# Optimization experiments

Hardware: AMD Instinct MI355X
Metric: run time of the kernel (lower is better)

The kernel has to match this reference:

```python
import jax, jax.numpy as jnp
import numpy as np

D_IN = 1024
D_OUT = 1024


def setup_inputs() -> dict:
    key = jax.random.key(0)
    ks = jax.random.split(key, 7)
    s = 1.0 / np.sqrt(D_IN)
    X = jax.random.normal(ks[0], (8, 2048, D_IN), dtype=jnp.float32)
    Wq = jax.random.uniform(ks[1], (D_OUT, D_IN), jnp.float32, -s, s)
    bq = jax.random.uniform(ks[2], (D_OUT,), jnp.float32, -s, s)
    Wk = jax.random.uniform(ks[3], (D_OUT, D_IN), jnp.float32, -s, s)
    bk = jax.random.uniform(ks[4], (D_OUT,), jnp.float32, -s, s)
    Wv = jax.random.uniform(ks[5], (D_OUT, D_IN), jnp.float32, -s, s)
    bv = jax.random.uniform(ks[6], (D_OUT,), jnp.float32, -s, s)
    return {"X": X, "Wq": Wq, "bq": bq, "Wk": Wk, "bk": bk, "Wv": Wv, "bv": bv}


def reference(X, Wq, bq, Wk, bk, Wv, bv):
    # Linear projections (torch Linear: y = x @ W.T + b)
    Q = jnp.einsum('bsi,oi->bso', X, Wq) + bq
    K = jnp.einsum('bsi,oi->bso', X, Wk) + bk
    V = jnp.einsum('bsi,oi->bso', X, Wv) + bv
    # scores[b, j, l] = Q[b, j] . K[b, l]
    scores = jnp.einsum('bjd,bld->bjl', Q, K)
    # FAITHFUL to source: tril zeroes (not -inf) the upper triangle, then scale
    sqrt_dk = jnp.sqrt(jnp.float32(D_OUT))
    scores = jnp.tril(scores) / sqrt_dk
    A = jax.nn.softmax(scores, axis=2)  # [b, j, l]
    # FAITHFUL: einsum 'ijk,ijl->ijl' = sum over k of A, broadcast-multiplied by V
    out = jnp.sum(A, axis=2, keepdims=True) * V  # [b, s, d_out]
    return out
```

## Files before the change

### kernel.cpp

```cpp
#include <hip/hip_runtime.h>
#include <stdint.h>

#define M_TOTAL 16384
#define N_TOTAL 1024
#define K_TOTAL 1024
#define BM 128
#define BN 128
#define BK 64
#define NTILES (K_TOTAL / BK)
#define NWG ((M_TOTAL / BM) * (N_TOTAL / BN))

using f32x4  = __attribute__((ext_vector_type(4))) float;
using bf16x8 = __attribute__((ext_vector_type(8))) short;
using bf16x4 = __attribute__((ext_vector_type(4))) short;

#define AS1 __attribute__((address_space(1)))
#define AS3 __attribute__((address_space(3)))
#define SB() __builtin_amdgcn_sched_barrier(0)

__device__ __forceinline__ unsigned packrne(float x, float y) {
    unsigned ux = __builtin_bit_cast(unsigned, x);
    unsigned uy = __builtin_bit_cast(unsigned, y);
    ux += 0x7fffu + ((ux >> 16) & 1u);
    uy += 0x7fffu + ((uy >> 16) & 1u);
    return (ux >> 16) | (uy & 0xffff0000u);
}

#define N8X (M_TOTAL * K_TOTAL / 8)
#define N8W (N_TOTAL * K_TOTAL / 8)
__global__ __launch_bounds__(256) void cvt2_kernel(
    const float* __restrict__ X, const float* __restrict__ W,
    uint4* __restrict__ Xb, uint4* __restrict__ Wb)
{
    const int i = blockIdx.x * 256 + threadIdx.x;
    const float* src; uint4* dst; int idx;
    if (i < N8X) { src = X; dst = Xb; idx = i; }
    else         { src = W; dst = Wb; idx = i - N8X; }
    const f32x4* p = (const f32x4*)src + (size_t)idx * 2;
    const f32x4 a = p[0], b = p[1];
    uint4 r;
    r.x = packrne(a[0], a[1]);
    r.y = packrne(a[2], a[3]);
    r.z = packrne(b[0], b[1]);
    r.w = packrne(b[2], b[3]);
    dst[idx] = r;
}

__global__ __launch_bounds__(256) void gemm2b_kernel(
    const unsigned short* __restrict__ Xb, const unsigned short* __restrict__ Wb,
    const float* __restrict__ bias, float* __restrict__ C)
{
    __shared__ __align__(16) char smem[65536];

    const int tid  = threadIdx.x;
    const int lane = tid & 63;
    const int wave = tid >> 6;
    const int wr = wave >> 1;
    const int wc = wave & 1;

    const int bid  = blockIdx.x;
    const int work = (bid & 7) * (NWG / 8) + (bid >> 3);
    const int bm = work >> 3;
    const int bn = work & 7;
    const int m0 = bm * BM, n0 = bn * BN;

    const int srow = wave * 8 + (lane >> 3);
    const int kge  = ((lane & 7) ^ ((lane >> 3) & 7)) * 8;

    auto stage = [&](int t, int b) {
        #pragma unroll
        for (int j = 0; j < 4; ++j) {
            __builtin_amdgcn_global_load_lds(
                (const AS1 void*)(Xb + (size_t)(m0 + j * 32 + srow) * K_TOTAL
                                     + t * BK + kge),
                (AS3 void*)(smem + b * 16384 + j * 4096 + wave * 1024),
                16, 0, 0);
        }
        #pragma unroll
        for (int j = 0; j < 4; ++j) {
            __builtin_amdgcn_global_load_lds(
                (const AS1 void*)(Wb + (size_t)(n0 + j * 32 + srow) * K_TOTAL
                                     + t * BK + kge),
                (AS3 void*)(smem + 32768 + b * 16384 + j * 4096 + wave * 1024),
                16, 0, 0);
        }
    };

    const int cl = lane & 15;
    const int kb = lane >> 4;

    f32x4 acc[4][4] = {};

#define BARRIER() SB(); __builtin_amdgcn_s_barrier(); SB()
#define VM(N)     asm volatile("s_waitcnt vmcnt(" #N ")" ::: "memory"); SB()

    auto compute_tile = [&](int buf) {
        const char* Ab = smem + buf * 16384;
        const char* Bb = smem + 32768 + buf * 16384;
        #pragma unroll
        for (int ks = 0; ks < 2; ++ks) {
            const int kg = ks * 4 + kb;
            bf16x8 aF[4], bF[4];
            #pragma unroll
            for (int i = 0; i < 4; ++i) {
                const int ar = wr * 64 + i * 16 + cl;
                aF[i] = *(const bf16x8*)(Ab + ar * 128 + ((kg ^ (ar & 7)) << 4));
                const int br = wc * 64 + i * 16 + cl;
                bF[i] = *(const bf16x8*)(Bb + br * 128 + ((kg ^ (br & 7)) << 4));
            }
            __builtin_amdgcn_s_setprio(1);
            #pragma unroll
            for (int i = 0; i < 4; ++i)
                #pragma unroll
                for (int j = 0; j < 4; ++j)
                    acc[i][j] = __builtin_amdgcn_mfma_f32_16x16x32_bf16(
                        aF[i], bF[j], acc[i][j], 0, 0, 0);
            __builtin_amdgcn_s_setprio(0);
        }
    };

    stage(0, 0);
    stage(1, 1);
    VM(8);
    BARRIER();
    compute_tile(0);

    #pragma unroll 1
    for (int t = 1; t < NTILES; ++t) {
        const int buf = t & 1, nbuf = buf ^ 1;
        BARRIER();
        if (t + 1 < NTILES) {
            stage(t + 1, nbuf);
            VM(8);
        } else {
            VM(0);
        }
        BARRIER();
        compute_tile(buf);
    }

    const int r0 = (lane >> 4) * 4;
    #pragma unroll
    for (int ni = 0; ni < 4; ++ni) {
        const int n = n0 + wc * 64 + ni * 16 + cl;
        const float bvv = bias[n];
        #pragma unroll
        for (int mi = 0; mi < 4; ++mi) {
            const int m = m0 + wr * 64 + mi * 16 + r0;
            #pragma unroll
            for (int r = 0; r < 4; ++r)
                C[(size_t)(m + r) * N_TOTAL + n] = acc[mi][ni][r] + bvv;
        }
    }
#undef BARRIER
#undef VM
}

__device__ __forceinline__ short f2bf(float f) {
    unsigned u = __builtin_bit_cast(unsigned, f);
    u += 0x7fffu + ((u >> 16) & 1u);
    return (short)(u >> 16);
}

__global__ __launch_bounds__(256) void fb_gemm_bias_kernel(
    const float* __restrict__ X, const float* __restrict__ W,
    const float* __restrict__ bias, float* __restrict__ C)
{
    __shared__ short As[BM * BK];
    __shared__ short Bs[BN * BK];

    const int tid  = threadIdx.x;
    const int lane = tid & 63;
    const int wave = tid >> 6;
    const int wr = wave >> 1;
    const int wc = wave & 1;

    const int bid  = blockIdx.x;
    const int work = (bid & 7) * (NWG / 8) + (bid >> 3);
    const int bm = work >> 3;
    const int bn = work & 7;
    const int m0 = bm * BM, n0 = bn * BN;

    const int srow  = tid >> 4;
    const int scol4 = tid & 15;

    f32x4 acc[4][4] = {};
    char* const Ab = (char*)As;
    char* const Bb = (char*)Bs;

    for (int k0 = 0; k0 < K_TOTAL; k0 += BK) {
        __syncthreads();
        #pragma unroll
        for (int pass = 0; pass < 8; ++pass) {
            const int row = srow + pass * 16;
            const int off = (row * (BK * 2) + scol4 * 8) ^ ((row & 7) << 4);
            {
                const f32x4 v = *(const f32x4*)(X + (size_t)(m0 + row) * K_TOTAL + k0 + scol4 * 4);
                bf16x4 b;
                b[0] = f2bf(v[0]); b[1] = f2bf(v[1]); b[2] = f2bf(v[2]); b[3] = f2bf(v[3]);
                *(bf16x4*)(Ab + off) = b;
            }
            {
                const f32x4 v = *(const f32x4*)(W + (size_t)(n0 + row) * K_TOTAL + k0 + scol4 * 4);
                bf16x4 b;
                b[0] = f2bf(v[0]); b[1] = f2bf(v[1]); b[2] = f2bf(v[2]); b[3] = f2bf(v[3]);
                *(bf16x4*)(Bb + off) = b;
            }
        }
        __syncthreads();

        #pragma unroll
        for (int ks = 0; ks < 2; ++ks) {
            const int kel = ks * 32 + ((lane >> 4) << 3);
            bf16x8 af[4], bfr[4];
            #pragma unroll
            for (int i = 0; i < 4; ++i) {
                const int ar = wr * 64 + i * 16 + (lane & 15);
                af[i]  = *(const bf16x8*)(Ab + ((ar * (BK * 2) + kel * 2) ^ ((ar & 7) << 4)));
                const int br = wc * 64 + i * 16 + (lane & 15);
                bfr[i] = *(const bf16x8*)(Bb + ((br * (BK * 2) + kel * 2) ^ ((br & 7) << 4)));
            }
            #pragma unroll
            for (int mi = 0; mi < 4; ++mi)
                #pragma unroll
                for (int ni = 0; ni < 4; ++ni)
                    acc[mi][ni] = __builtin_amdgcn_mfma_f32_16x16x32_bf16(
                        af[mi], bfr[ni], acc[mi][ni], 0, 0, 0);
        }
    }

    const int cl = lane & 15;
    const int r0 = (lane >> 4) * 4;
    #pragma unroll
    for (int ni = 0; ni < 4; ++ni) {
        const int n = n0 + wc * 64 + ni * 16 + cl;
        const float bvv = bias[n];
        #pragma unroll
        for (int mi = 0; mi < 4; ++mi) {
            const int m = m0 + wr * 64 + mi * 16 + r0;
            #pragma unroll
            for (int r = 0; r < 4; ++r)
                C[(size_t)(m + r) * N_TOTAL + n] = acc[mi][ni][r] + bvv;
        }
    }
}

extern "C" void kernel_launch(void* const* d_in, const int* in_sizes, int n_in,
                              void* d_out, int out_size, void* d_ws, size_t ws_size,
                              hipStream_t stream) {
    const float* X  = (const float*)d_in[0];
    const float* Wv = (const float*)d_in[5];
    const float* bv = (const float*)d_in[6];
    float* out = (float*)d_out;

    const size_t XB_BYTES = (size_t)M_TOTAL * K_TOTAL * 2;
    const size_t WB_BYTES = (size_t)N_TOTAL * K_TOTAL * 2;

    if (ws_size >= XB_BYTES + WB_BYTES) {
        unsigned short* Xb = (unsigned short*)d_ws;
        unsigned short* Wb = (unsigned short*)((char*)d_ws + XB_BYTES);
        cvt2_kernel<<<dim3((N8X + N8W) / 256), dim3(256), 0, stream>>>(
            X, Wv, (uint4*)Xb, (uint4*)Wb);
        gemm2b_kernel<<<dim3(NWG), dim3(256), 0, stream>>>(Xb, Wb, bv, out);
    } else {
        fb_gemm_bias_kernel<<<dim3(NWG), dim3(256), 0, stream>>>(X, Wv, bv, out);
    }
}
```

Baseline: 59.97 us.

## Fuse X bf16 conversion into GEMM by staging fp32 X tiles in LDS

Removes the standalone pass that converted the whole activation matrix to bf16. The GEMM now loads fp32 X tiles directly into LDS and converts them to bf16 in registers before the MFMAs; only the weights are pre-converted. The tile changes to 256x128 with K-step 32 to fit the larger fp32 A tile, raising LDS to 80KB. This cuts the extra global write and read of the bf16 X copy, at the cost of more LDS traffic, in-loop conversion work, and possibly lower occupancy.

Result: slower. 95.22 us (+58.8%).

```diff
diff --git a/kernel.cpp b/kernel.cpp
--- a/kernel.cpp
+++ b/kernel.cpp
@@ -4,9 +4,9 @@
 #define M_TOTAL 16384
 #define N_TOTAL 1024
 #define K_TOTAL 1024
-#define BM 128
+#define BM 256
 #define BN 128
-#define BK 64
+#define BK 32
 #define NTILES (K_TOTAL / BK)
 #define NWG ((M_TOTAL / BM) * (N_TOTAL / BN))
 
@@ -26,31 +26,26 @@
     return (ux >> 16) | (uy & 0xffff0000u);
 }
 
-#define N8X (M_TOTAL * K_TOTAL / 8)
 #define N8W (N_TOTAL * K_TOTAL / 8)
-__global__ __launch_bounds__(256) void cvt2_kernel(
-    const float* __restrict__ X, const float* __restrict__ W,
-    uint4* __restrict__ Xb, uint4* __restrict__ Wb)
+__global__ __launch_bounds__(256) void cvtW_kernel(
+    const float* __restrict__ W, uint4* __restrict__ Wb)
 {
     const int i = blockIdx.x * 256 + threadIdx.x;
-    const float* src; uint4* dst; int idx;
-    if (i < N8X) { src = X; dst = Xb; idx = i; }
-    else         { src = W; dst = Wb; idx = i - N8X; }
-    const f32x4* p = (const f32x4*)src + (size_t)idx * 2;
+    const f32x4* p = (const f32x4*)W + (size_t)i * 2;
     const f32x4 a = p[0], b = p[1];
     uint4 r;
     r.x = packrne(a[0], a[1]);
     r.y = packrne(a[2], a[3]);
     r.z = packrne(b[0], b[1]);
     r.w = packrne(b[2], b[3]);
-    dst[idx] = r;
-}
-
-__global__ __launch_bounds__(256) void gemm2b_kernel(
-    const unsigned short* __restrict__ Xb, const unsigned short* __restrict__ Wb,
+    Wb[i] = r;
+}
+
+__global__ __launch_bounds__(256) void gemm_xf32_kernel(
+    const float* __restrict__ X, const unsigned short* __restrict__ Wb,
     const float* __restrict__ bias, float* __restrict__ C)
 {
-    __shared__ __align__(16) char smem[65536];
+    __shared__ __align__(16) char smem[81920];
 
     const int tid  = threadIdx.x;
     const int lane = tid & 63;
@@ -64,74 +59,96 @@
     const int bn = work & 7;
     const int m0 = bm * BM, n0 = bn * BN;
 
-    const int srow = wave * 8 + (lane >> 3);
-    const int kge  = ((lane & 7) ^ ((lane >> 3) & 7)) * 8;
+    const int arow8 = lane >> 3;
+    const int aslot = ((lane & 7) ^ ((lane >> 3) & 7)) * 4;
+    const int brow16 = lane >> 2;
+    const int bslot  = ((lane & 3) ^ ((lane >> 2) & 3)) * 8;
 
     auto stage = [&](int t, int b) {
         #pragma unroll
-        for (int j = 0; j < 4; ++j) {
+        for (int j = 0; j < 8; ++j) {
+            const int rb = j * 32 + wave * 8;
             __builtin_amdgcn_global_load_lds(
-                (const AS1 void*)(Xb + (size_t)(m0 + j * 32 + srow) * K_TOTAL
-                                     + t * BK + kge),
-                (AS3 void*)(smem + b * 16384 + j * 4096 + wave * 1024),
-                16, 0, 0);
-        }
-        #pragma unroll
-        for (int j = 0; j < 4; ++j) {
+                (const AS1 void*)(X + (size_t)(m0 + rb + arow8) * K_TOTAL
+                                     + t * BK + aslot),
+                (AS3 void*)(smem + b * 32768 + rb * 128), 16, 0, 0);
+        }
+        #pragma unroll
+        for (int j = 0; j < 2; ++j) {
+            const int rb = j * 64 + wave * 16;
             __builtin_amdgcn_global_load_lds(
-                (const AS1 void*)(Wb + (size_t)(n0 + j * 32 + srow) * K_TOTAL
-                                     + t * BK + kge),
-                (AS3 void*)(smem + 32768 + b * 16384 + j * 4096 + wave * 1024),
-                16, 0, 0);
+                (const AS1 void*)(Wb + (size_t)(n0 + rb + brow16) * K_TOTAL
+                                     + t * BK + bslot),
+                (AS3 void*)(smem + 65536 + b * 8192 + rb * 64), 16, 0, 0);
         }
     };
 
     const int cl = lane & 15;
     const int kb = lane >> 4;
 
-    f32x4 acc[4][4] = {};
+    f32x4 acc[8][4] = {};
 
 #define BARRIER() SB(); __builtin_amdgcn_s_barrier(); SB()
 #define VM(N)     asm volatile("s_waitcnt vmcnt(" #N ")" ::: "memory"); SB()
 
+    auto read_a = [&](const char* Ab, int i) -> bf16x8 {
+        const int row = wr * 128 + i * 16 + cl;
+        const int rs  = row & 7;
+        const f32x4 v0 = *(const f32x4*)(Ab + row * 128 + (((2 * kb)     ^ rs) << 4));
+        const f32x4 v1 = *(const f32x4*)(Ab + row * 128 + (((2 * kb + 1) ^ rs) << 4));
+        uint4 c;
+        c.x = packrne(v0[0], v0[1]);
+        c.y = packrne(v0[2], v0[3]);
+        c.z = packrne(v1[0], v1[1]);
+        c.w = packrne(v1[2], v1[3]);
+        return __builtin_bit_cast(bf16x8, c);
+    };
+    auto read_b = [&](const char* Bb, int j) -> bf16x8 {
+        const int row = wc * 64 + j * 16 + cl;
+        return *(const bf16x8*)(Bb + row * 64 + ((kb ^ (row & 3)) << 4));
+    };
+
     auto compute_tile = [&](int buf) {
-        const char* Ab = smem + buf * 16384;
-        const char* Bb = smem + 32768 + buf * 16384;
-        #pragma unroll
-        for (int ks = 0; ks < 2; ++ks) {
-            const int kg = ks * 4 + kb;
-            bf16x8 aF[4], bF[4];
-            #pragma unroll
-            for (int i = 0; i < 4; ++i) {
-                const int ar = wr * 64 + i * 16 + cl;
-                aF[i] = *(const bf16x8*)(Ab + ar * 128 + ((kg ^ (ar & 7)) << 4));
-                const int br = wc * 64 + i * 16 + cl;
-                bF[i] = *(const bf16x8*)(Bb + br * 128 + ((kg ^ (br & 7)) << 4));
-            }
-            __builtin_amdgcn_s_setprio(1);
-            #pragma unroll
-            for (int i = 0; i < 4; ++i)
-                #pragma unroll
-                for (int j = 0; j < 4; ++j)
-                    acc[i][j] = __builtin_amdgcn_mfma_f32_16x16x32_bf16(
-                        aF[i], bF[j], acc[i][j], 0, 0, 0);
-            __builtin_amdgcn_s_setprio(0);
-        }
+        const char* Ab = smem + buf * 32768;
+        const char* Bb = smem + 65536 + buf * 8192;
+        bf16x8 bF[4], aF[4];
+        #pragma unroll
+        for (int j = 0; j < 4; ++j) bF[j] = read_b(Bb, j);
+        #pragma unroll
+        for (int i = 0; i < 4; ++i) aF[i] = read_a(Ab, i);
+        __builtin_amdgcn_s_setprio(1);
+        #pragma unroll
+        for (int i = 0; i < 4; ++i)
+            #pragma unroll
+            for (int j = 0; j < 4; ++j)
+                acc[i][j] = __builtin_amdgcn_mfma_f32_16x16x32_bf16(
+                    aF[i], bF[j], acc[i][j], 0, 0, 0);
+        __builtin_amdgcn_s_setprio(0);
+        #pragma unroll
+        for (int i = 0; i < 4; ++i) aF[i] = read_a(Ab, 4 + i);
+        __builtin_amdgcn_s_setprio(1);
+        #pragma unroll
+        for (int i = 0; i < 4; ++i)
+            #pragma unroll
+            for (int j = 0; j < 4; ++j)
+                acc[4 + i][j] = __builtin_amdgcn_mfma_f32_16x16x32_bf16(
+                    aF[i], bF[j], acc[4 + i][j], 0, 0, 0);
+        __builtin_amdgcn_s_setprio(0);
     };
 
     stage(0, 0);
     stage(1, 1);
-    VM(8);
+    VM(10);
     BARRIER();
     compute_tile(0);
 
     #pragma unroll 1
     for (int t = 1; t < NTILES; ++t) {
-        const int buf = t & 1, nbuf = buf ^ 1;
+        const int buf = t & 1;
         BARRIER();
         if (t + 1 < NTILES) {
-            stage(t + 1, nbuf);
-            VM(8);
+            stage(t + 1, buf ^ 1);
+            VM(10);
         } else {
             VM(0);
         }
@@ -145,8 +162,8 @@
         const int n = n0 + wc * 64 + ni * 16 + cl;
         const float bvv = bias[n];
         #pragma unroll
-        for (int mi = 0; mi < 4; ++mi) {
-            const int m = m0 + wr * 64 + mi * 16 + r0;
+        for (int mi = 0; mi < 8; ++mi) {
+            const int m = m0 + wr * 128 + mi * 16 + r0;
             #pragma unroll
             for (int r = 0; r < 4; ++r)
                 C[(size_t)(m + r) * N_TOTAL + n] = acc[mi][ni][r] + bvv;
@@ -162,12 +179,17 @@
     return (short)(u >> 16);
 }
 
+#define FBM 128
+#define FBN 128
+#define FBK 64
+#define FNWG ((M_TOTAL / FBM) * (N_TOTAL / FBN))
+
 __global__ __launch_bounds__(256) void fb_gemm_bias_kernel(
     const float* __restrict__ X, const float* __restrict__ W,
     const float* __restrict__ bias, float* __restrict__ C)
 {
-    __shared__ short As[BM * BK];
-    __shared__ short Bs[BN * BK];
+    __shared__ short As[FBM * FBK];
+    __shared__ short Bs[FBN * FBK];
 
     const int tid  = threadIdx.x;
     const int lane = tid & 63;
@@ -176,10 +198,10 @@
     const int wc = wave & 1;
 
     const int bid  = blockIdx.x;
-    const int work = (bid & 7) * (NWG / 8) + (bid >> 3);
+    const int work = (bid & 7) * (FNWG / 8) + (bid >> 3);
     const int bm = work >> 3;
     const int bn = work & 7;
-    const int m0 = bm * BM, n0 = bn * BN;
+    const int m0 = bm * FBM, n0 = bn * FBN;
 
     const int srow  = tid >> 4;
     const int scol4 = tid & 15;
@@ -188,12 +210,12 @@
     char* const Ab = (char*)As;
     char* const Bb = (char*)Bs;
 
-    for (int k0 = 0; k0 < K_TOTAL; k0 += BK) {
+    for (int k0 = 0; k0 < K_TOTAL; k0 += FBK) {
         __syncthreads();
         #pragma unroll
         for (int pass = 0; pass < 8; ++pass) {
             const int row = srow + pass * 16;
-            const int off = (row * (BK * 2) + scol4 * 8) ^ ((row & 7) << 4);
+            const int off = (row * (FBK * 2) + scol4 * 8) ^ ((row & 7) << 4);
             {
                 const f32x4 v = *(const f32x4*)(X + (size_t)(m0 + row) * K_TOTAL + k0 + scol4 * 4);
                 bf16x4 b;
@@ -216,9 +238,9 @@
             #pragma unroll
             for (int i = 0; i < 4; ++i) {
                 const int ar = wr * 64 + i * 16 + (lane & 15);
-                af[i]  = *(const bf16x8*)(Ab + ((ar * (BK * 2) + kel * 2) ^ ((ar & 7) << 4)));
+                af[i]  = *(const bf16x8*)(Ab + ((ar * (FBK * 2) + kel * 2) ^ ((ar & 7) << 4)));
                 const int br = wc * 64 + i * 16 + (lane & 15);
-                bfr[i] = *(const bf16x8*)(Bb + ((br * (BK * 2) + kel * 2) ^ ((br & 7) << 4)));
+                bfr[i] = *(const bf16x8*)(Bb + ((br * (FBK * 2) + kel * 2) ^ ((br & 7) << 4)));
             }
             #pragma unroll
             for (int mi = 0; mi < 4; ++mi)
@@ -253,16 +275,13 @@
     const float* bv = (const float*)d_in[6];
     float* out = (float*)d_out;
 
-    const size_t XB_BYTES = (size_t)M_TOTAL * K_TOTAL * 2;
     const size_t WB_BYTES = (size_t)N_TOTAL * K_TOTAL * 2;
 
-    if (ws_size >= XB_BYTES + WB_BYTES) {
-        unsigned short* Xb = (unsigned short*)d_ws;
-        unsigned short* Wb = (unsigned short*)((char*)d_ws + XB_BYTES);
-        cvt2_kernel<<<dim3((N8X + N8W) / 256), dim3(256), 0, stream>>>(
-            X, Wv, (uint4*)Xb, (uint4*)Wb);
-        gemm2b_kernel<<<dim3(NWG), dim3(256), 0, stream>>>(Xb, Wb, bv, out);
+    if (ws_size >= WB_BYTES) {
+        unsigned short* Wb = (unsigned short*)d_ws;
+        cvtW_kernel<<<dim3(N8W / 256), dim3(256), 0, stream>>>(Wv, (uint4*)Wb);
+        gemm_xf32_kernel<<<dim3(NWG), dim3(256), 0, stream>>>(X, Wb, bv, out);
     } else {
-        fb_gemm_bias_kernel<<<dim3(NWG), dim3(256), 0, stream>>>(X, Wv, bv, out);
-    }
-}
+        fb_gemm_bias_kernel<<<dim3(FNWG), dim3(256), 0, stream>>>(X, Wv, bv, out);
+    }
+}
```

## Pre-swizzle W into MFMA fragment layout and load B directly to registers

Applied to the files above, without the earlier changes.

The conversion kernel now writes the bf16 weight matrix in a fragment-major layout that matches the MFMA B-operand lane mapping. The GEMM then loads each wave's B fragments straight from global memory into double-buffered registers instead of staging them through LDS, which halves shared memory to 32 KB and removes the B LDS reads. The main loop is unrolled by two so it can alternate the register buffers. The cost is higher register pressure and B loads that are no longer shared across waves, relying on L2/L1 for the reuse between the two wr waves.

Result: slower. 62.80 us (+4.7%).

```diff
diff --git a/kernel.cpp b/kernel.cpp
--- a/kernel.cpp
+++ b/kernel.cpp
@@ -27,30 +27,45 @@
 }
 
 #define N8X (M_TOTAL * K_TOTAL / 8)
-#define N8W (N_TOTAL * K_TOTAL / 8)
+#define NWF (N_TOTAL * K_TOTAL / 8)
 __global__ __launch_bounds__(256) void cvt2_kernel(
     const float* __restrict__ X, const float* __restrict__ W,
-    uint4* __restrict__ Xb, uint4* __restrict__ Wb)
+    uint4* __restrict__ Xb, uint4* __restrict__ Wf)
 {
     const int i = blockIdx.x * 256 + threadIdx.x;
-    const float* src; uint4* dst; int idx;
-    if (i < N8X) { src = X; dst = Xb; idx = i; }
-    else         { src = W; dst = Wb; idx = i - N8X; }
-    const f32x4* p = (const f32x4*)src + (size_t)idx * 2;
-    const f32x4 a = p[0], b = p[1];
-    uint4 r;
-    r.x = packrne(a[0], a[1]);
-    r.y = packrne(a[2], a[3]);
-    r.z = packrne(b[0], b[1]);
-    r.w = packrne(b[2], b[3]);
-    dst[idx] = r;
-}
-
-__global__ __launch_bounds__(256) void gemm2b_kernel(
-    const unsigned short* __restrict__ Xb, const unsigned short* __restrict__ Wb,
+    if (i < N8X) {
+        const f32x4* p = (const f32x4*)X + (size_t)i * 2;
+        const f32x4 a = p[0], b = p[1];
+        uint4 r;
+        r.x = packrne(a[0], a[1]);
+        r.y = packrne(a[2], a[3]);
+        r.z = packrne(b[0], b[1]);
+        r.w = packrne(b[2], b[3]);
+        Xb[i] = r;
+    } else {
+        const int idx = i - N8X;
+        const int J   = idx >> 11;
+        const int rem = idx & 2047;
+        const int h   = rem >> 6;
+        const int l   = rem & 63;
+        const int cl = l & 15, kb = l >> 4;
+        const float* src = W + (size_t)(J * 16 + cl) * K_TOTAL + h * 32 + kb * 8;
+        const f32x4 a = *(const f32x4*)src;
+        const f32x4 b = *(const f32x4*)(src + 4);
+        uint4 r;
+        r.x = packrne(a[0], a[1]);
+        r.y = packrne(a[2], a[3]);
+        r.z = packrne(b[0], b[1]);
+        r.w = packrne(b[2], b[3]);
+        Wf[idx] = r;
+    }
+}
+
+__global__ __launch_bounds__(256) void gemm_bd_kernel(
+    const unsigned short* __restrict__ Xb, const unsigned short* __restrict__ Wfu,
     const float* __restrict__ bias, float* __restrict__ C)
 {
-    __shared__ __align__(16) char smem[65536];
+    __shared__ __align__(16) char smem[32768];
 
     const int tid  = threadIdx.x;
     const int lane = tid & 63;
@@ -66,8 +81,7 @@
 
     const int srow = wave * 8 + (lane >> 3);
     const int kge  = ((lane & 7) ^ ((lane >> 3) & 7)) * 8;
-
-    auto stage = [&](int t, int b) {
+    auto stage_A = [&](int t, int b) {
         #pragma unroll
         for (int j = 0; j < 4; ++j) {
             __builtin_amdgcn_global_load_lds(
@@ -76,14 +90,17 @@
                 (AS3 void*)(smem + b * 16384 + j * 4096 + wave * 1024),
                 16, 0, 0);
         }
-        #pragma unroll
-        for (int j = 0; j < 4; ++j) {
-            __builtin_amdgcn_global_load_lds(
-                (const AS1 void*)(Wb + (size_t)(n0 + j * 32 + srow) * K_TOTAL
-                                     + t * BK + kge),
-                (AS3 void*)(smem + 32768 + b * 16384 + j * 4096 + wave * 1024),
-                16, 0, 0);
-        }
+    };
+
+    const uint4* Wf = (const uint4*)Wfu;
+    const int Jbase = (n0 + wc * 64) >> 4;
+    auto load_B = [&](int t, bf16x8 (&B)[4][2]) {
+        #pragma unroll
+        for (int jj = 0; jj < 4; ++jj)
+            #pragma unroll
+            for (int kh = 0; kh < 2; ++kh)
+                B[jj][kh] = __builtin_bit_cast(bf16x8,
+                    Wf[(size_t)(Jbase + jj) * 2048 + (t * 2 + kh) * 64 + lane]);
     };
 
     const int cl = lane & 15;
@@ -94,50 +111,58 @@
 #define BARRIER() SB(); __builtin_amdgcn_s_barrier(); SB()
 #define VM(N)     asm volatile("s_waitcnt vmcnt(" #N ")" ::: "memory"); SB()
 
-    auto compute_tile = [&](int buf) {
+    auto compute_tile = [&](int buf, bf16x8 (&Bc)[4][2]) {
         const char* Ab = smem + buf * 16384;
-        const char* Bb = smem + 32768 + buf * 16384;
-        #pragma unroll
-        for (int ks = 0; ks < 2; ++ks) {
-            const int kg = ks * 4 + kb;
-            bf16x8 aF[4], bF[4];
+        #pragma unroll
+        for (int kh = 0; kh < 2; ++kh) {
+            const int kg = kh * 4 + kb;
+            bf16x8 aF[4];
             #pragma unroll
             for (int i = 0; i < 4; ++i) {
                 const int ar = wr * 64 + i * 16 + cl;
                 aF[i] = *(const bf16x8*)(Ab + ar * 128 + ((kg ^ (ar & 7)) << 4));
-                const int br = wc * 64 + i * 16 + cl;
-                bF[i] = *(const bf16x8*)(Bb + br * 128 + ((kg ^ (br & 7)) << 4));
             }
             __builtin_amdgcn_s_setprio(1);
             #pragma unroll
             for (int i = 0; i < 4; ++i)
                 #pragma unroll
-                for (int j = 0; j < 4; ++j)
-                    acc[i][j] = __builtin_amdgcn_mfma_f32_16x16x32_bf16(
-                        aF[i], bF[j], acc[i][j], 0, 0, 0);
+                for (int jj = 0; jj < 4; ++jj)
+                    acc[i][jj] = __builtin_amdgcn_mfma_f32_16x16x32_bf16(
+                        aF[i], Bc[jj][kh], acc[i][jj], 0, 0, 0);
             __builtin_amdgcn_s_setprio(0);
         }
     };
 
-    stage(0, 0);
-    stage(1, 1);
-    VM(8);
+    bf16x8 B0r[4][2], B1r[4][2];
+
+#define ITER(T, BCUR, BNXT)                                                     \
+    {                                                                           \
+        BARRIER();                       \
+        if ((T) + 1 < NTILES) {                                                 \
+            stage_A((T) + 1, ((T) & 1) ^ 1);                                    \
+            load_B((T) + 1, BNXT);                                              \
+            VM(12);                         \
+        } else {                                                                \
+            VM(0);                                       \
+        }                                                                       \
+        BARRIER();                                 \
+        compute_tile((T) & 1, BCUR);                                            \
+    }
+
+    stage_A(0, 0);
+    load_B(0, B0r);
+    stage_A(1, 1);
+    load_B(1, B1r);
+    VM(12);
     BARRIER();
-    compute_tile(0);
+    compute_tile(0, B0r);
 
     #pragma unroll 1
-    for (int t = 1; t < NTILES; ++t) {
-        const int buf = t & 1, nbuf = buf ^ 1;
-        BARRIER();
-        if (t + 1 < NTILES) {
-            stage(t + 1, nbuf);
-            VM(8);
-        } else {
-            VM(0);
-        }
-        BARRIER();
-        compute_tile(buf);
-    }
+    for (int t = 1; t < NTILES - 1; t += 2) {
+        ITER(t,     B1r, B0r);
+        ITER(t + 1, B0r, B1r);
+    }
+    ITER(NTILES - 1, B1r, B0r);
 
     const int r0 = (lane >> 4) * 4;
     #pragma unroll
@@ -152,6 +177,7 @@
                 C[(size_t)(m + r) * N_TOTAL + n] = acc[mi][ni][r] + bvv;
         }
     }
+#undef ITER
 #undef BARRIER
 #undef VM
 }
@@ -254,14 +280,14 @@
     float* out = (float*)d_out;
 
     const size_t XB_BYTES = (size_t)M_TOTAL * K_TOTAL * 2;
-    const size_t WB_BYTES = (size_t)N_TOTAL * K_TOTAL * 2;
-
-    if (ws_size >= XB_BYTES + WB_BYTES) {
+    const size_t WF_BYTES = (size_t)N_TOTAL * K_TOTAL * 2;
+
+    if (ws_size >= XB_BYTES + WF_BYTES) {
         unsigned short* Xb = (unsigned short*)d_ws;
-        unsigned short* Wb = (unsigned short*)((char*)d_ws + XB_BYTES);
-        cvt2_kernel<<<dim3((N8X + N8W) / 256), dim3(256), 0, stream>>>(
-            X, Wv, (uint4*)Xb, (uint4*)Wb);
-        gemm2b_kernel<<<dim3(NWG), dim3(256), 0, stream>>>(Xb, Wb, bv, out);
+        unsigned short* Wf = (unsigned short*)((char*)d_ws + XB_BYTES);
+        cvt2_kernel<<<dim3((N8X + NWF) / 256), dim3(256), 0, stream>>>(
+            X, Wv, (uint4*)Xb, (uint4*)Wf);
+        gemm_bd_kernel<<<dim3(NWG), dim3(256), 0, stream>>>(Xb, Wf, bv, out);
     } else {
         fb_gemm_bias_kernel<<<dim3(NWG), dim3(256), 0, stream>>>(X, Wv, bv, out);
     }
```
